# Kernel tuning notes

Measured on AMD Instinct MI355X. Metric: run time of the kernel, lower is better.

## Reference

```python
import jax, jax.numpy as jnp
import numpy as np

# decoded layout constants
NN, NO, SD = 16, 8, 4          # num_neighbors, num_obstacles, state_dim_per_agent
B = 131072                      # batch rows
H1, E, HP, AD = 64, 16, 64, 2   # phi hidden, embed, psi hidden, action dim
D_ROBOT, D_OBST = 0.3, 0.3
B_GAMMA, B_EXPH = 0.05, 1.0
PHI_MIN, PHI_MAX = -2.0, 2.0
A_MAX = 2.0


def setup_inputs() -> dict:
    key = jax.random.key(0)
    kx, kw = jax.random.split(key)
    # x: [count | goal(SD) | NN neighbor rel-states (SD each) | NO obstacle rel-pos (2 each)]
    x = jax.random.normal(kx, (B, 1 + SD + SD * NN + 2 * NO), dtype=jnp.float32) * 2.0
    x = x.at[:, 0].set(float(NN))
    names = [("Wp1n", (SD, H1)), ("bp1n", (H1,)), ("Wp2n", (H1, E)), ("bp2n", (E,)),
             ("Wr1n", (E, H1)), ("br1n", (H1,)), ("Wr2n", (H1, E)), ("br2n", (E,)),
             ("Wp1o", (2, H1)), ("bp1o", (H1,)), ("Wp2o", (H1, E)), ("bp2o", (E,)),
             ("Wr1o", (E, H1)), ("br1o", (H1,)), ("Wr2o", (H1, E)), ("br2o", (E,)),
             ("Wpsi1", (2 * E + SD, HP)), ("bpsi1", (HP,)), ("Wpsi2", (HP, AD)), ("bpsi2", (AD,))]
    ks = jax.random.split(kw, len(names))
    inp = {"x": x}
    for (n, sh), k in zip(names, ks):
        s = 1.0 / np.sqrt(sh[0])  # torch Linear default init scale
        inp[n] = jax.random.uniform(k, sh, jnp.float32, -s, s)
    return inp


def _mlp2(h, W1, b1, W2, b2):
    # Feedforward: activation between layers, linear output
    return jax.nn.relu(h @ W1 + b1) @ W2 + b2


def _deepset(el, Wp1, bp1, Wp2, bp2, Wr1, br1, Wr2, br2):
    # el: [B, n, d] -> phi each element, sum over set, rho
    phi = _mlp2(el, Wp1, bp1, Wp2, bp2)          # [B, n, E]
    return _mlp2(phi.sum(axis=1), Wr1, br1, Wr2, br2)  # [B, E]


def _barrier_sum(P, D):
    # P: [B, n, 2]; APF barrier gamma * P / (|P| * (|P|-D)^exph), summed over n
    nrm = jnp.linalg.norm(P, axis=-1, keepdims=True)   # [B, n, 1]
    H = nrm - D
    return (B_GAMMA * P / (nrm * H ** B_EXPH)).sum(axis=1)  # [B, 2]


def reference(x, Wp1n, bp1n, Wp2n, bp2n, Wr1n, br1n, Wr2n, br2n,
              Wp1o, bp1o, Wp2o, bp2o, Wr1o, br1o, Wr2o, br2o,
              Wpsi1, bpsi1, Wpsi2, bpsi2):
    nb = x.shape[0]
    g = x[:, 1:1 + SD]                                        # goal
    nbr = x[:, 1 + SD:1 + SD + SD * NN].reshape(nb, NN, SD)   # neighbor rel-states
    obs = x[:, 1 + SD + SD * NN:].reshape(nb, NO, 2)          # obstacle rel-pos

    rho_n = _deepset(nbr, Wp1n, bp1n, Wp2n, bp2n, Wr1n, br1n, Wr2n, br2n)
    rho_o = _deepset(obs, Wp1o, bp1o, Wp2o, bp2o, Wr1o, br1o, Wr2o, br2o)

    h = jnp.concatenate([rho_n, rho_o, g], axis=1)            # [B, 2E+SD]
    emp = _mlp2(h, Wpsi1, bpsi1, Wpsi2, bpsi2)                # psi network
    emp = (jnp.tanh(emp) + 1.0) / 2.0 * (PHI_MAX - PHI_MIN) + PHI_MIN  # scale_empty

    bar = _barrier_sum(-nbr[:, :, :2], D_ROBOT) + _barrier_sum(-obs, D_OBST)

    action = emp + bar
    # scale(): divide rows whose inf-norm exceeds a_max
    inv_alpha = jnp.maximum(jnp.max(jnp.abs(action), axis=1, keepdims=True) / A_MAX, 1.0)
    return action / inv_alpha
```

## Files before the change

### kernel.cpp

```cpp
#include <hip/hip_runtime.h>
#include <math.h>


typedef __attribute__((ext_vector_type(8))) _Float16 f16x8;
typedef __attribute__((ext_vector_type(2))) __fp16 fp16x2;
typedef __attribute__((ext_vector_type(4))) float f32x4;

#define XW 85
#define WPB 8

#define FR_S1N  0
#define FR_S1O  4
#define FR_G2N  8
#define FR_G2O  10
#define FR_RNA  12
#define FR_RNB  16
#define FR_ROA  18
#define FR_ROB  22
#define FR_PSI1 24
#define FR_PSI2 32
#define N_FRAGS 34

#define BIG_STR 144
#define PHI_STR 80
#define CAT_STR 144
#define L_BIG 0
#define L_PHI 2304
#define L_CAT 3584
#define L_OUT 5888
#define L_BAR 6016
#define WAVE_LDS 6144

__device__ __forceinline__ float fast_rcp(float x)  { return __builtin_amdgcn_rcpf(x); }
__device__ __forceinline__ float fast_sqrt(float x) { return __builtin_amdgcn_sqrtf(x); }

__device__ __forceinline__ float two_tanh(float a) {
    float ax = fabsf(a);
    float e = __expf(2.0f * ax);
    float t = 1.0f - 2.0f * fast_rcp(e + 1.0f);
    return copysignf(2.0f * t, a);
}

__device__ __forceinline__ void lds_order() {
    __asm__ __volatile__("" ::: "memory");
}

__device__ __forceinline__ unsigned pk2(float a, float b) {
    union { fp16x2 h; unsigned u; } t;
    t.h = __builtin_amdgcn_cvt_pkrtz(a, b);
    return t.u;
}
__device__ __forceinline__ f16x8 make_a4(float f0, float f1, float f2, float f3) {
    union { unsigned u[4]; f16x8 v; } U;
    U.u[0] = pk2(f0, f1); U.u[1] = pk2(f2, f3); U.u[2] = 0; U.u[3] = 0;
    return U.v;
}
__device__ __forceinline__ f16x8 make_a2(float f0, float f1) {
    union { unsigned u[4]; f16x8 v; } U;
    U.u[0] = pk2(f0, f1); U.u[1] = 0; U.u[2] = 0; U.u[3] = 0;
    return U.v;
}
__device__ __forceinline__ f16x8 lds_af(const char* area, int stride, int off, int lane) {
    int mm = lane & 15, qq = lane >> 4;
    return *(const f16x8*)(area + mm * stride + off + qq * 16);
}
__device__ __forceinline__ f16x8 load_bh(const _Float16* wsf, int frag, int lane) {
    return ((const f16x8*)(wsf + (size_t)frag * 512))[lane];
}
__device__ __forceinline__ f32x4 cinit(float b) {
    f32x4 c; c[0] = b; c[1] = b; c[2] = b; c[3] = b; return c;
}
__device__ __forceinline__ f32x4 mfma1(f16x8 a, f16x8 b, f32x4 c) {
    return __builtin_amdgcn_mfma_f32_16x16x32_f16(a, b, c, 0, 0, 0);
}

__global__ void bn_prep(const float* __restrict__ Wp1n, const float* __restrict__ Wp2n,
                        const float* __restrict__ Wr1n, const float* __restrict__ Wr2n,
                        const float* __restrict__ Wp1o, const float* __restrict__ Wp2o,
                        const float* __restrict__ Wr1o, const float* __restrict__ Wr2o,
                        const float* __restrict__ Wpsi1, const float* __restrict__ Wpsi2,
                        _Float16* __restrict__ wsf)
{
    int f = blockIdx.x;
    int lane = threadIdx.x;
    const float* W; int K, N, kk = 0, nt = 0, rel;
    if (f < 4)        { W = Wp1n;  K = 4;  N = 64; nt = f; }
    else if (f < 8)   { W = Wp1o;  K = 2;  N = 64; nt = f - 4; }
    else if (f < 10)  { W = Wp2n;  K = 64; N = 16; kk = f - 8; }
    else if (f < 12)  { W = Wp2o;  K = 64; N = 16; kk = f - 10; }
    else if (f < 16)  { W = Wr1n;  K = 16; N = 64; nt = f - 12; }
    else if (f < 18)  { W = Wr2n;  K = 64; N = 16; kk = f - 16; }
    else if (f < 22)  { W = Wr1o;  K = 16; N = 64; nt = f - 18; }
    else if (f < 24)  { W = Wr2o;  K = 64; N = 16; kk = f - 22; }
    else if (f < 32)  { rel = f - 24; W = Wpsi1; K = 36; N = 64; kk = rel >> 2; nt = rel & 3; }
    else              { W = Wpsi2; K = 64; N = 2;  kk = f - 32; }

    int q = lane >> 4, c = lane & 15;
    _Float16* dst = wsf + (size_t)f * 512 + lane * 8;
    for (int j = 0; j < 8; ++j) {
        int k = kk * 32 + q * 8 + j;
        int n = nt * 16 + c;
        float v = (k < K && n < N) ? W[k * N + n] : 0.f;
        dst[j] = (_Float16)v;
    }
}

__global__ __launch_bounds__(512) void bn_main(
    const float* __restrict__ x, const _Float16* __restrict__ wsf,
    const float* __restrict__ bp1n, const float* __restrict__ bp2n,
    const float* __restrict__ br1n, const float* __restrict__ br2n,
    const float* __restrict__ bp1o, const float* __restrict__ bp2o,
    const float* __restrict__ br1o, const float* __restrict__ br2o,
    const float* __restrict__ bpsi1, const float* __restrict__ bpsi2,
    float* __restrict__ out, int nb)
{
    __shared__ char smem[WPB * WAVE_LDS];
    const int lane = threadIdx.x & 63;
    const int wid  = threadIdx.x >> 6;
    const int group = blockIdx.x * WPB + wid;
    const int row0 = group * 16;
    if (row0 >= nb) return;

    char* Wl   = smem + wid * WAVE_LDS;
    char* BIG  = Wl + L_BIG;
    char* PHI  = Wl + L_PHI;
    char* CAT  = Wl + L_CAT;
    char* OUTA = Wl + L_OUT;
    char* BAR  = Wl + L_BAR;

    const int m = lane & 15, q = lane >> 4, c = m;
    const bool q1b = (q & 1), q2b = (q & 2);

    for (int i = lane; i < 128; i += 64) {
        int r = i >> 3, d = i & 7;
        *(unsigned*)(PHI + r * PHI_STR + 32 + d * 4) = 0;
    }
    for (int i = lane; i < 256; i += 64) {
        int r = i >> 4, d = i & 15;
        *(unsigned*)(CAT + r * CAT_STR + 64 + d * 4) = 0;
    }
    lds_order();

    {
        const float* xb = x + (size_t)(row0 + m) * XW;
        float bx = 0.f, by = 0.f;
        #pragma unroll
        for (int i = 0; i < 4; ++i) {
            int n = 4 * q + i;
            float px = -xb[5 + 4 * n], py = -xb[6 + 4 * n];
            float nrm = fast_sqrt(px * px + py * py);
            float coef = 0.05f * fast_rcp(nrm * (nrm - 0.3f));
            bx = fmaf(coef, px, bx);
            by = fmaf(coef, py, by);
        }
        #pragma unroll
        for (int i = 0; i < 2; ++i) {
            int o = 2 * q + i;
            float px = -xb[69 + 2 * o], py = -xb[70 + 2 * o];
            float nrm = fast_sqrt(px * px + py * py);
            float coef = 0.05f * fast_rcp(nrm * (nrm - 0.3f));
            bx = fmaf(coef, px, bx);
            by = fmaf(coef, py, by);
        }
        bx += __shfl_xor(bx, 16); by += __shfl_xor(by, 16);
        bx += __shfl_xor(bx, 32); by += __shfl_xor(by, 32);
        if (q == 0) { float2 bb; bb.x = bx; bb.y = by; *(float2*)(BAR + m * 8) = bb; }
    }

    if (lane < 16) {
        const float* xr = x + (size_t)(row0 + lane) * XW;
        uint2 gv;
        gv.x = pk2(xr[1], xr[2]);
        gv.y = pk2(xr[3], xr[4]);
        *(uint2*)(CAT + lane * CAT_STR + 64) = gv;
    }

    float b_s1n[4], b_s1o[4], b_rna[4], b_roa[4], b_p1[4];
    #pragma unroll
    for (int nt = 0; nt < 4; ++nt) {
        b_s1n[nt] = bp1n[nt * 16 + c];
        b_s1o[nt] = bp1o[nt * 16 + c];
        b_rna[nt] = br1n[nt * 16 + c];
        b_roa[nt] = br1o[nt * 16 + c];
        b_p1[nt]  = bpsi1[nt * 16 + c];
    }
    float b_g2n = 16.f * bp2n[c];
    float b_g2o = 8.f * bp2o[c];
    float b_rnb = br2n[c];
    float b_rob = br2o[c];
    float b_p2  = (c < 2) ? bpsi2[c] : 0.f;

    f16x8 Bs1n[4], Bg2n[2];
    #pragma unroll
    for (int nt = 0; nt < 4; ++nt) Bs1n[nt] = load_bh(wsf, FR_S1N + nt, lane);
    Bg2n[0] = load_bh(wsf, FR_G2N + 0, lane);
    Bg2n[1] = load_bh(wsf, FR_G2N + 1, lane);

    {
        float buf[4][4];
        #pragma unroll
        for (int i = 0; i < 4; ++i) {
            const float* xi = x + (size_t)(row0 + i) * XW + 5 + 4 * m;
            buf[i][0] = xi[0]; buf[i][1] = xi[1]; buf[i][2] = xi[2]; buf[i][3] = xi[3];
        }
        #pragma unroll 4
        for (int r = 0; r < 16; ++r) {
            int sl = r & 3;
            f16x8 A = make_a4(buf[sl][0], buf[sl][1], buf[sl][2], buf[sl][3]);
            if (r + 4 < 16) {
                const float* xn = x + (size_t)(row0 + r + 4) * XW + 5 + 4 * m;
                buf[sl][0] = xn[0]; buf[sl][1] = xn[1];
                buf[sl][2] = xn[2]; buf[sl][3] = xn[3];
            }
            float sv[4];
            #pragma unroll
            for (int nt = 0; nt < 4; ++nt) {
                f32x4 cc = mfma1(A, Bs1n[nt], cinit(b_s1n[nt]));
                float s = fmaxf(cc[0], 0.f) + fmaxf(cc[1], 0.f)
                        + fmaxf(cc[2], 0.f) + fmaxf(cc[3], 0.f);
                s += __shfl_xor(s, 16);
                s += __shfl_xor(s, 32);
                sv[nt] = s;
            }
            float w = q2b ? (q1b ? sv[3] : sv[2]) : (q1b ? sv[1] : sv[0]);
            *(_Float16*)(BIG + r * BIG_STR + (q * 16 + c) * 2) = (_Float16)w;
        }
    }
    f16x8 Brna[4];
    #pragma unroll
    for (int nt = 0; nt < 4; ++nt) Brna[nt] = load_bh(wsf, FR_RNA + nt, lane);
    lds_order();

    {
        f16x8 A0 = lds_af(BIG, BIG_STR, 0, lane);
        f16x8 A1 = lds_af(BIG, BIG_STR, 64, lane);
        f32x4 ca = mfma1(A0, Bg2n[0], cinit(b_g2n));
        f32x4 cb = mfma1(A1, Bg2n[1], cinit(0.f));
        #pragma unroll
        for (int reg = 0; reg < 4; ++reg)
            *(_Float16*)(PHI + (q * 4 + reg) * PHI_STR + c * 2) = (_Float16)(ca[reg] + cb[reg]);
    }
    f16x8 Brnb[2], Bs1o[4];
    Brnb[0] = load_bh(wsf, FR_RNB + 0, lane);
    Brnb[1] = load_bh(wsf, FR_RNB + 1, lane);
    #pragma unroll
    for (int nt = 0; nt < 4; ++nt) Bs1o[nt] = load_bh(wsf, FR_S1O + nt, lane);
    lds_order();

    {
        f16x8 A = lds_af(PHI, PHI_STR, 0, lane);
        #pragma unroll
        for (int nt = 0; nt < 4; ++nt) {
            f32x4 cc = mfma1(A, Brna[nt], cinit(b_rna[nt]));
            #pragma unroll
            for (int reg = 0; reg < 4; ++reg)
                *(_Float16*)(BIG + (q * 4 + reg) * BIG_STR + (nt * 16 + c) * 2) = (_Float16)fmaxf(cc[reg], 0.f);
        }
    }
    f16x8 Bg2o[2];
    Bg2o[0] = load_bh(wsf, FR_G2O + 0, lane);
    Bg2o[1] = load_bh(wsf, FR_G2O + 1, lane);
    float of0[8], of1[8];
    #pragma unroll
    for (int t = 0; t < 8; ++t) {
        const float* xo = x + (size_t)(row0 + 2 * t + (m >> 3)) * XW + 69 + 2 * (m & 7);
        of0[t] = xo[0]; of1[t] = xo[1];
    }
    lds_order();

    {
        f16x8 A0 = lds_af(BIG, BIG_STR, 0, lane);
        f16x8 A1 = lds_af(BIG, BIG_STR, 64, lane);
        f32x4 ca = mfma1(A0, Brnb[0], cinit(b_rnb));
        f32x4 cb = mfma1(A1, Brnb[1], cinit(0.f));
        #pragma unroll
        for (int reg = 0; reg < 4; ++reg)
            *(_Float16*)(CAT + (q * 4 + reg) * CAT_STR + c * 2) = (_Float16)(ca[reg] + cb[reg]);
    }
    f16x8 Broa[4];
    #pragma unroll
    for (int nt = 0; nt < 4; ++nt) Broa[nt] = load_bh(wsf, FR_ROA + nt, lane);
    lds_order();

    {
        #pragma unroll
        for (int t = 0; t < 8; ++t) {
            f16x8 A = make_a2(of0[t], of1[t]);
            float sv[4];
            #pragma unroll
            for (int nt = 0; nt < 4; ++nt) {
                f32x4 cc = mfma1(A, Bs1o[nt], cinit(b_s1o[nt]));
                float s = fmaxf(cc[0], 0.f) + fmaxf(cc[1], 0.f)
                        + fmaxf(cc[2], 0.f) + fmaxf(cc[3], 0.f);
                s += __shfl_xor(s, 16);
                sv[nt] = s;
            }
            float w1 = q1b ? sv[1] : sv[0];
            float w2 = q1b ? sv[3] : sv[2];
            char* p = BIG + (2 * t + (q >> 1)) * BIG_STR + ((q & 1) * 16 + c) * 2;
            *(_Float16*)(p)      = (_Float16)w1;
            *(_Float16*)(p + 64) = (_Float16)w2;
        }
    }
    f16x8 Brob[2];
    Brob[0] = load_bh(wsf, FR_ROB + 0, lane);
    Brob[1] = load_bh(wsf, FR_ROB + 1, lane);
    lds_order();

    {
        f16x8 A0 = lds_af(BIG, BIG_STR, 0, lane);
        f16x8 A1 = lds_af(BIG, BIG_STR, 64, lane);
        f32x4 ca = mfma1(A0, Bg2o[0], cinit(b_g2o));
        f32x4 cb = mfma1(A1, Bg2o[1], cinit(0.f));
        #pragma unroll
        for (int reg = 0; reg < 4; ++reg)
            *(_Float16*)(PHI + (q * 4 + reg) * PHI_STR + c * 2) = (_Float16)(ca[reg] + cb[reg]);
    }
    f16x8 Bp1a[4];
    #pragma unroll
    for (int nt = 0; nt < 4; ++nt) Bp1a[nt] = load_bh(wsf, FR_PSI1 + nt, lane);
    lds_order();

    {
        f16x8 A = lds_af(PHI, PHI_STR, 0, lane);
        #pragma unroll
        for (int nt = 0; nt < 4; ++nt) {
            f32x4 cc = mfma1(A, Broa[nt], cinit(b_roa[nt]));
            #pragma unroll
            for (int reg = 0; reg < 4; ++reg)
                *(_Float16*)(BIG + (q * 4 + reg) * BIG_STR + (nt * 16 + c) * 2) = (_Float16)fmaxf(cc[reg], 0.f);
        }
    }
    f16x8 Bp1b[4], Bp2[2];
    #pragma unroll
    for (int nt = 0; nt < 4; ++nt) Bp1b[nt] = load_bh(wsf, FR_PSI1 + 4 + nt, lane);
    Bp2[0] = load_bh(wsf, FR_PSI2 + 0, lane);
    Bp2[1] = load_bh(wsf, FR_PSI2 + 1, lane);
    lds_order();

    {
        f16x8 A0 = lds_af(BIG, BIG_STR, 0, lane);
        f16x8 A1 = lds_af(BIG, BIG_STR, 64, lane);
        f32x4 ca = mfma1(A0, Brob[0], cinit(b_rob));
        f32x4 cb = mfma1(A1, Brob[1], cinit(0.f));
        #pragma unroll
        for (int reg = 0; reg < 4; ++reg)
            *(_Float16*)(CAT + (q * 4 + reg) * CAT_STR + (16 + c) * 2) = (_Float16)(ca[reg] + cb[reg]);
    }
    lds_order();

    {
        f16x8 A0 = lds_af(CAT, CAT_STR, 0, lane);
        f16x8 A1 = lds_af(CAT, CAT_STR, 64, lane);
        #pragma unroll
        for (int nt = 0; nt < 4; ++nt) {
            f32x4 ca = mfma1(A0, Bp1a[nt], cinit(b_p1[nt]));
            f32x4 cb = mfma1(A1, Bp1b[nt], cinit(0.f));
            #pragma unroll
            for (int reg = 0; reg < 4; ++reg)
                *(_Float16*)(BIG + (q * 4 + reg) * BIG_STR + (nt * 16 + c) * 2) = (_Float16)fmaxf(ca[reg] + cb[reg], 0.f);
        }
    }
    lds_order();

    {
        f16x8 A0 = lds_af(BIG, BIG_STR, 0, lane);
        f16x8 A1 = lds_af(BIG, BIG_STR, 64, lane);
        f32x4 ca = mfma1(A0, Bp2[0], cinit(b_p2));
        f32x4 cb = mfma1(A1, Bp2[1], cinit(0.f));
        if (c < 2) {
            #pragma unroll
            for (int reg = 0; reg < 4; ++reg)
                *(float*)(OUTA + (q * 4 + reg) * 8 + c * 4) = ca[reg] + cb[reg];
        }
    }
    lds_order();

    if (lane < 16) {
        float2 a  = *(const float2*)(OUTA + lane * 8);
        float2 bb = *(const float2*)(BAR + lane * 8);
        float a0 = two_tanh(a.x) + bb.x;
        float a1 = two_tanh(a.y) + bb.y;
        float amax = fmaxf(fabsf(a0), fabsf(a1));
        float inv_alpha = fmaxf(amax * 0.5f, 1.0f);
        float rr = fast_rcp(inv_alpha);
        float2 o; o.x = a0 * rr; o.y = a1 * rr;
        *(float2*)(out + (size_t)(row0 + lane) * 2) = o;
    }
}

extern "C" void kernel_launch(void* const* d_in, const int* in_sizes, int n_in,
                              void* d_out, int out_size, void* d_ws, size_t ws_size,
                              hipStream_t stream) {
    const float* x     = (const float*)d_in[0];
    const float* Wp1n  = (const float*)d_in[1];
    const float* bp1n  = (const float*)d_in[2];
    const float* Wp2n  = (const float*)d_in[3];
    const float* bp2n  = (const float*)d_in[4];
    const float* Wr1n  = (const float*)d_in[5];
    const float* br1n  = (const float*)d_in[6];
    const float* Wr2n  = (const float*)d_in[7];
    const float* br2n  = (const float*)d_in[8];
    const float* Wp1o  = (const float*)d_in[9];
    const float* bp1o  = (const float*)d_in[10];
    const float* Wp2o  = (const float*)d_in[11];
    const float* bp2o  = (const float*)d_in[12];
    const float* Wr1o  = (const float*)d_in[13];
    const float* br1o  = (const float*)d_in[14];
    const float* Wr2o  = (const float*)d_in[15];
    const float* br2o  = (const float*)d_in[16];
    const float* Wpsi1 = (const float*)d_in[17];
    const float* bpsi1 = (const float*)d_in[18];
    const float* Wpsi2 = (const float*)d_in[19];
    const float* bpsi2 = (const float*)d_in[20];
    float* out = (float*)d_out;

    int nb = in_sizes[0] / XW;
    _Float16* wsf = (_Float16*)d_ws;

    bn_prep<<<N_FRAGS, 64, 0, stream>>>(Wp1n, Wp2n, Wr1n, Wr2n,
                                        Wp1o, Wp2o, Wr1o, Wr2o,
                                        Wpsi1, Wpsi2, wsf);

    int groups = (nb + 15) / 16;
    int blocks = (groups + WPB - 1) / WPB;
    bn_main<<<blocks, 512, 0, stream>>>(x, wsf,
                                        bp1n, bp2n, br1n, br2n,
                                        bp1o, bp2o, br1o, br2o,
                                        bpsi1, bpsi2, out, nb);
}
```

Baseline: 165.5 us.

## Swap MFMA roles so the set-sum accumulates in registers, and halve block size

Result: faster. 156.3 us (-5.5%).

```diff
diff --git a/kernel.cpp b/kernel.cpp
--- a/kernel.cpp
+++ b/kernel.cpp
@@ -7,7 +7,7 @@
 typedef __attribute__((ext_vector_type(4))) float f32x4;
 
 #define XW 85
-#define WPB 8
+#define WPB 4
 
 #define FR_S1N  0
 #define FR_S1O  4
@@ -105,7 +105,7 @@
     }
 }
 
-__global__ __launch_bounds__(512) void bn_main(
+__global__ __launch_bounds__(256) void bn_main(
     const float* __restrict__ x, const _Float16* __restrict__ wsf,
     const float* __restrict__ bp1n, const float* __restrict__ bp2n,
     const float* __restrict__ br1n, const float* __restrict__ br2n,
@@ -129,7 +129,7 @@
     char* BAR  = Wl + L_BAR;
 
     const int m = lane & 15, q = lane >> 4, c = m;
-    const bool q1b = (q & 1), q2b = (q & 2);
+    const float* xrow = x + (size_t)(row0 + m) * XW;
 
     for (int i = lane; i < 128; i += 64) {
         int r = i >> 3, d = i & 7;
@@ -142,12 +142,11 @@
     lds_order();
 
     {
-        const float* xb = x + (size_t)(row0 + m) * XW;
         float bx = 0.f, by = 0.f;
         #pragma unroll
         for (int i = 0; i < 4; ++i) {
             int n = 4 * q + i;
-            float px = -xb[5 + 4 * n], py = -xb[6 + 4 * n];
+            float px = -xrow[5 + 4 * n], py = -xrow[6 + 4 * n];
             float nrm = fast_sqrt(px * px + py * py);
             float coef = 0.05f * fast_rcp(nrm * (nrm - 0.3f));
             bx = fmaf(coef, px, bx);
@@ -156,7 +155,7 @@
         #pragma unroll
         for (int i = 0; i < 2; ++i) {
             int o = 2 * q + i;
-            float px = -xb[69 + 2 * o], py = -xb[70 + 2 * o];
+            float px = -xrow[69 + 2 * o], py = -xrow[70 + 2 * o];
             float nrm = fast_sqrt(px * px + py * py);
             float coef = 0.05f * fast_rcp(nrm * (nrm - 0.3f));
             bx = fmaf(coef, px, bx);
@@ -197,34 +196,33 @@
     Bg2n[1] = load_bh(wsf, FR_G2N + 1, lane);
 
     {
-        float buf[4][4];
-        #pragma unroll
-        for (int i = 0; i < 4; ++i) {
-            const float* xi = x + (size_t)(row0 + i) * XW + 5 + 4 * m;
-            buf[i][0] = xi[0]; buf[i][1] = xi[1]; buf[i][2] = xi[2]; buf[i][3] = xi[3];
-        }
+        f32x4 acc[4];
+        #pragma unroll
+        for (int nt = 0; nt < 4; ++nt) acc[nt] = cinit(0.f);
+        float p0 = xrow[5], p1 = xrow[6], p2 = xrow[7], p3 = xrow[8];
         #pragma unroll 4
-        for (int r = 0; r < 16; ++r) {
-            int sl = r & 3;
-            f16x8 A = make_a4(buf[sl][0], buf[sl][1], buf[sl][2], buf[sl][3]);
-            if (r + 4 < 16) {
-                const float* xn = x + (size_t)(row0 + r + 4) * XW + 5 + 4 * m;
-                buf[sl][0] = xn[0]; buf[sl][1] = xn[1];
-                buf[sl][2] = xn[2]; buf[sl][3] = xn[3];
+        for (int mm = 0; mm < 16; ++mm) {
+            float n0, n1, n2, n3;
+            if (mm + 1 < 16) {
+                const float* xn = xrow + 5 + 4 * (mm + 1);
+                n0 = xn[0]; n1 = xn[1]; n2 = xn[2]; n3 = xn[3];
             }
-            float sv[4];
+            f16x8 A = make_a4(p0, p1, p2, p3);
             #pragma unroll
             for (int nt = 0; nt < 4; ++nt) {
                 f32x4 cc = mfma1(A, Bs1n[nt], cinit(b_s1n[nt]));
-                float s = fmaxf(cc[0], 0.f) + fmaxf(cc[1], 0.f)
-                        + fmaxf(cc[2], 0.f) + fmaxf(cc[3], 0.f);
-                s += __shfl_xor(s, 16);
-                s += __shfl_xor(s, 32);
-                sv[nt] = s;
+                #pragma unroll
+                for (int reg = 0; reg < 4; ++reg)
+                    acc[nt][reg] += fmaxf(cc[reg], 0.f);
             }
-            float w = q2b ? (q1b ? sv[3] : sv[2]) : (q1b ? sv[1] : sv[0]);
-            *(_Float16*)(BIG + r * BIG_STR + (q * 16 + c) * 2) = (_Float16)w;
-        }
+            if (mm + 1 < 16) { p0 = n0; p1 = n1; p2 = n2; p3 = n3; }
+        }
+        #pragma unroll
+        for (int nt = 0; nt < 4; ++nt)
+            #pragma unroll
+            for (int reg = 0; reg < 4; ++reg)
+                *(_Float16*)(BIG + (q * 4 + reg) * BIG_STR + (nt * 16 + c) * 2)
+                    = (_Float16)acc[nt][reg];
     }
     f16x8 Brna[4];
     #pragma unroll
@@ -260,12 +258,6 @@
     f16x8 Bg2o[2];
     Bg2o[0] = load_bh(wsf, FR_G2O + 0, lane);
     Bg2o[1] = load_bh(wsf, FR_G2O + 1, lane);
-    float of0[8], of1[8];
-    #pragma unroll
-    for (int t = 0; t < 8; ++t) {
-        const float* xo = x + (size_t)(row0 + 2 * t + (m >> 3)) * XW + 69 + 2 * (m & 7);
-        of0[t] = xo[0]; of1[t] = xo[1];
-    }
     lds_order();
 
     {
@@ -283,24 +275,26 @@
     lds_order();
 
     {
-        #pragma unroll
-        for (int t = 0; t < 8; ++t) {
-            f16x8 A = make_a2(of0[t], of1[t]);
-            float sv[4];
+        f32x4 acc[4];
+        #pragma unroll
+        for (int nt = 0; nt < 4; ++nt) acc[nt] = cinit(0.f);
+        #pragma unroll
+        for (int oo = 0; oo < 8; ++oo) {
+            f16x8 A = make_a2(xrow[69 + 2 * oo], xrow[70 + 2 * oo]);
             #pragma unroll
             for (int nt = 0; nt < 4; ++nt) {
                 f32x4 cc = mfma1(A, Bs1o[nt], cinit(b_s1o[nt]));
-                float s = fmaxf(cc[0], 0.f) + fmaxf(cc[1], 0.f)
-                        + fmaxf(cc[2], 0.f) + fmaxf(cc[3], 0.f);
-                s += __shfl_xor(s, 16);
-                sv[nt] = s;
+                #pragma unroll
+                for (int reg = 0; reg < 4; ++reg)
+                    acc[nt][reg] += fmaxf(cc[reg], 0.f);
             }
-            float w1 = q1b ? sv[1] : sv[0];
-            float w2 = q1b ? sv[3] : sv[2];
-            char* p = BIG + (2 * t + (q >> 1)) * BIG_STR + ((q & 1) * 16 + c) * 2;
-            *(_Float16*)(p)      = (_Float16)w1;
-            *(_Float16*)(p + 64) = (_Float16)w2;
-        }
+        }
+        #pragma unroll
+        for (int nt = 0; nt < 4; ++nt)
+            #pragma unroll
+            for (int reg = 0; reg < 4; ++reg)
+                *(_Float16*)(BIG + (q * 4 + reg) * BIG_STR + (nt * 16 + c) * 2)
+                    = (_Float16)acc[nt][reg];
     }
     f16x8 Brob[2];
     Brob[0] = load_bh(wsf, FR_ROB + 0, lane);
@@ -424,7 +418,7 @@
 
     int groups = (nb + 15) / 16;
     int blocks = (groups + WPB - 1) / WPB;
-    bn_main<<<blocks, 512, 0, stream>>>(x, wsf,
+    bn_main<<<blocks, 256, 0, stream>>>(x, wsf,
                                         bp1n, bp2n, br1n, br2n,
                                         bp1o, bp2o, br1o, br2o,
                                         bpsi1, bpsi2, out, nb);
```
